# Performance work log

Measured on AMD Instinct MI355X. Metric: run time of the kernel, lower is better.

Reference implementation:

```python
import jax, jax.numpy as jnp
import numpy as np


def setup_inputs() -> dict:
    key = jax.random.key(0)
    ks = jax.random.split(key, 8)
    B, N, K, C_in, M, C_add, C_out = 2, 40000, 16, 64, 16, 3, 128
    in_features = (C_in + C_add) * M  # 1072
    input_features = jax.random.normal(ks[0], (B, N, C_in), dtype=jnp.float32)
    neighbor_inds = jax.random.randint(ks[1], (B, N, K), 0, N, dtype=jnp.int64)
    inverse_neighbors = jax.random.randint(ks[2], (B, N * K), 0, N * K, dtype=jnp.int64)
    inverse_k = jax.random.randint(ks[3], (B, N * K), 0, K, dtype=jnp.int64)
    inverse_idx = jax.random.randint(ks[4], (B, N * K), 0, N, dtype=jnp.int64)
    weightnet = jax.random.normal(ks[5], (B, N, K, M), dtype=jnp.float32)
    additional_features = jax.random.normal(ks[6], (B, N, K, C_add), dtype=jnp.float32)
    bound = 1.0 / np.sqrt(in_features)
    kw, kb = jax.random.split(ks[7])
    linear_weight = jax.random.uniform(kw, (C_out, in_features), dtype=jnp.float32, minval=-bound, maxval=bound)
    linear_bias = jax.random.uniform(kb, (C_out,), dtype=jnp.float32, minval=-bound, maxval=bound)
    return {
        "input_features": input_features,
        "neighbor_inds": neighbor_inds,
        "inverse_neighbors": inverse_neighbors,
        "inverse_k": inverse_k,
        "inverse_idx": inverse_idx,
        "weightnet": weightnet,
        "additional_features": additional_features,
        "linear_weight": linear_weight,
        "linear_bias": linear_bias,
    }


def reference(input_features, neighbor_inds, inverse_neighbors, inverse_k, inverse_idx,
              weightnet, additional_features, linear_weight, linear_bias):
    # inverse_* tensors are only used by the custom CUDA backward; unused here.
    B, N, K = neighbor_inds.shape
    # gather neighbor features: [B, N, K, C_in]
    gathered = jnp.take_along_axis(input_features[:, :, None, :],
                                   neighbor_inds[..., None], axis=1)
    # concat extra per-neighbor features -> [B, N, K, C]
    feats = jnp.concatenate([gathered, additional_features], axis=-1)
    # PConv: [B,N,C,K] @ [B,N,K,M] -> [B,N,C,M] -> flatten to [B,N,C*M]
    pconv = jnp.einsum('bnkc,bnkm->bncm', feats, weightnet)
    pconv = pconv.reshape(B, N, -1)
    # fused linear
    out = jnp.einsum('bnf,of->bno', pconv, linear_weight) + linear_bias
    return out
```

## Files before the change

kernel.cpp:

```cpp
#include <hip/hip_runtime.h>
#include <stdint.h>

typedef unsigned short u16;
typedef short short8 __attribute__((ext_vector_type(8)));
typedef float floatx4 __attribute__((ext_vector_type(4)));

#define NPERB   40000
#define NPTS    80000
#define KNBR    16
#define CIN     64
#define MDIM    16
#define CADD    3
#define CF      (CIN + CADD)
#define COUT    128
#define KF      1072
#define KP      1088
#define NKT     34
#define PTSB    16
#define SLAB    65
#define GRB     32
#define PPB     8
#define LROWB   2192

__device__ __forceinline__ u16 f2bf(float f) {
    union { float f; unsigned int u; } v; v.f = f;
    unsigned int u = v.u;
    return (u16)((u + 0x7FFFu + ((u >> 16) & 1u)) >> 16);
}
__device__ __forceinline__ short8 pack8(floatx4 x, floatx4 y) {
    union { short8 v; u16 a[8]; } u;
    u.a[0] = f2bf(x[0]); u.a[1] = f2bf(x[1]); u.a[2] = f2bf(x[2]); u.a[3] = f2bf(x[3]);
    u.a[4] = f2bf(y[0]); u.a[5] = f2bf(y[1]); u.a[6] = f2bf(y[2]); u.a[7] = f2bf(y[3]);
    return u.v;
}
__device__ __forceinline__ unsigned swz(unsigned chunk) {
    return chunk ^ ((chunk >> 3) & 7u);
}
__device__ __forceinline__ void gload_lds16(const void* g, void* l) {
    __builtin_amdgcn_global_load_lds(
        (const __attribute__((address_space(1))) void*)g,
        (__attribute__((address_space(3))) void*)l, 16, 0, 0);
}

__global__ void prep_lw_kernel(const float* __restrict__ lw, u16* __restrict__ lwp) {
    int i = blockIdx.x * 256 + threadIdx.x;
    if (i >= COUT * KP) return;
    int o = i / KP, f = i - o * KP;
    lwp[i] = (f < KF) ? f2bf(lw[(size_t)o * KF + f]) : (u16)0;
}

__device__ __forceinline__ void emit_point(
    int lane, float av, const float (&fv)[KNBR], const float* wl,
    u16* __restrict__ dst)
{
    const int em = lane & 15, ec = lane >> 4;
    float ev = 0.f;
#pragma unroll
    for (int k = 0; k < KNBR; k++)
        ev += __shfl(av, k * CADD + ec) * wl[k * MDIM + em];
    if (ec == 3) ev = 0.f;
    dst[1024 + lane] = f2bf(ev);

    floatx4 a0 = 0, a1 = 0, a2 = 0, a3 = 0;
#pragma unroll
    for (int k = 0; k < KNBR; k++) {
        const floatx4* w4 = (const floatx4*)(wl + k * MDIM);
        const float fvk = fv[k];
        a0 += fvk * w4[0]; a1 += fvk * w4[1];
        a2 += fvk * w4[2]; a3 += fvk * w4[3];
    }
    *(short8*)(dst + lane * 16)     = pack8(a0, a1);
    *(short8*)(dst + lane * 16 + 8) = pack8(a2, a3);
}

__global__ __launch_bounds__(256) void pconv_kernel(
    const float* __restrict__ inp,
    const int*   __restrict__ nbr,
    const float* __restrict__ wn,
    const float* __restrict__ addl,
    u16* __restrict__ pc)
{
    __shared__ __align__(16) float Wns[PPB * KNBR * MDIM];

    const int wave = threadIdx.x >> 6;
    const int lane = threadIdx.x & 63;
    const int pbase = blockIdx.x * PPB;
    const float* inpb = inp + ((pbase >= NPERB) ? (size_t)NPERB * CIN : 0);

    const int pr0 = wave * 2;
    const int p0  = __builtin_amdgcn_readfirstlane(pbase + pr0);
    const int p1  = p0 + 1;

    float* wl0 = Wns + pr0 * (KNBR * MDIM);
    float* wl1 = wl0 + KNBR * MDIM;
    gload_lds16(wn + (size_t)p0 * (KNBR * MDIM) + lane * 4, wl0);
    gload_lds16(wn + (size_t)p1 * (KNBR * MDIM) + lane * 4, wl1);

    float av0 = (lane < KNBR * CADD) ? addl[(size_t)p0 * (KNBR * CADD) + lane] : 0.f;
    float av1 = (lane < KNBR * CADD) ? addl[(size_t)p1 * (KNBR * CADD) + lane] : 0.f;

    const int* nb0 = nbr + (size_t)p0 * KNBR;
    const int* nb1 = nbr + (size_t)p1 * KNBR;
    int idx0[KNBR], idx1[KNBR];
#pragma unroll
    for (int k = 0; k < KNBR; k++) idx0[k] = nb0[k];
#pragma unroll
    for (int k = 0; k < KNBR; k++) idx1[k] = nb1[k];

    float fv0[KNBR], fv1[KNBR];
#pragma unroll
    for (int k = 0; k < KNBR; k++) fv0[k] = inpb[(size_t)idx0[k] * CIN + lane];
#pragma unroll
    for (int k = 0; k < KNBR; k++) fv1[k] = inpb[(size_t)idx1[k] * CIN + lane];

    asm volatile("s_waitcnt vmcnt(0)" ::: "memory");
    __builtin_amdgcn_sched_barrier(0);

    emit_point(lane, av0, fv0, wl0, pc + (size_t)p0 * KP);
    emit_point(lane, av1, fv1, wl1, pc + (size_t)p1 * KP);
}

__global__ __launch_bounds__(256) void gemm_kernel(
    const u16* __restrict__ pc,
    const u16* __restrict__ lwp,
    const float* __restrict__ bias,
    float* __restrict__ out)
{
    __shared__ __align__(16) u16 As[69 * 512];

    const int wave = threadIdx.x >> 6;
    const int lane = threadIdx.x & 63;
    const int r16 = lane & 15, quad = lane >> 4;
    const int rh = wave >> 1, ch = wave & 1;
    const int row0 = blockIdx.x * GRB;
    const int cb = ch * 64;

    const char* srcb = (const char*)pc + (size_t)row0 * (KP * 2);
#pragma unroll
    for (int j = 0; j < 18; j++) {
        const int w = j * 4 + wave;
        if (w < 69) {
            const unsigned d   = (unsigned)w * 1024u + (unsigned)lane * 16u;
            const unsigned row = d / (unsigned)LROWB;
            const unsigned col = d - row * (unsigned)LROWB;
            gload_lds16(srcb + (size_t)row * 2176u + col,
                        (char*)As + (size_t)w * 1024u);
        }
    }

    const u16* bB0 = lwp + (size_t)(cb + r16) * KP + quad * 8;
    const u16* bB1 = bB0 + (size_t)16 * KP;
    const u16* bB2 = bB0 + (size_t)32 * KP;
    const u16* bB3 = bB0 + (size_t)48 * KP;

    float bv[4];
#pragma unroll
    for (int n = 0; n < 4; n++) bv[n] = bias[cb + n * 16 + r16];

    const u16* aRd = As + (size_t)(rh * 16 + r16) * (LROWB / 2) + quad * 8;

    floatx4 acc[4];
#pragma unroll
    for (int n = 0; n < 4; n++) acc[n] = 0;

    short8 Bq[3][4];
    short8 AR0, AR1;

#define LOADB(t) { \
    Bq[(t) % 3][0] = *(const short8*)(bB0 + (t) * 32); \
    Bq[(t) % 3][1] = *(const short8*)(bB1 + (t) * 32); \
    Bq[(t) % 3][2] = *(const short8*)(bB2 + (t) * 32); \
    Bq[(t) % 3][3] = *(const short8*)(bB3 + (t) * 32); }

    LOADB(0)
    __builtin_amdgcn_sched_barrier(0);
    LOADB(1)
    __builtin_amdgcn_sched_barrier(0);

    asm volatile("s_waitcnt vmcnt(8)" ::: "memory");
    __syncthreads();
    AR0 = *(const short8*)aRd;

#define STEP(kt, NV, NL) { \
    if ((kt) + 2 < NKT) { LOADB((kt) + 2) __builtin_amdgcn_sched_barrier(0); } \
    if ((kt) + 1 < NKT) { \
        if ((((kt) + 1) & 1) == 0) AR0 = *(const short8*)(aRd + ((kt) + 1) * 32); \
        else                       AR1 = *(const short8*)(aRd + ((kt) + 1) * 32); \
    } \
    __builtin_amdgcn_sched_barrier(0); \
    asm volatile("s_waitcnt vmcnt(" #NV ") lgkmcnt(" #NL ")" ::: "memory"); \
    __builtin_amdgcn_sched_barrier(0); \
    _Pragma("unroll") \
    for (int n = 0; n < 4; n++) \
        acc[n] = __builtin_amdgcn_mfma_f32_16x16x32_bf16( \
            (((kt) & 1) == 0) ? AR0 : AR1, Bq[(kt) % 3][n], acc[n], 0, 0, 0); }

    STEP(0, 8, 1)  STEP(1, 8, 1)  STEP(2, 8, 1)  STEP(3, 8, 1)  STEP(4, 8, 1)
    STEP(5, 8, 1)  STEP(6, 8, 1)  STEP(7, 8, 1)  STEP(8, 8, 1)  STEP(9, 8, 1)
    STEP(10, 8, 1) STEP(11, 8, 1) STEP(12, 8, 1) STEP(13, 8, 1) STEP(14, 8, 1)
    STEP(15, 8, 1) STEP(16, 8, 1) STEP(17, 8, 1) STEP(18, 8, 1) STEP(19, 8, 1)
    STEP(20, 8, 1) STEP(21, 8, 1) STEP(22, 8, 1) STEP(23, 8, 1) STEP(24, 8, 1)
    STEP(25, 8, 1) STEP(26, 8, 1) STEP(27, 8, 1) STEP(28, 8, 1) STEP(29, 8, 1)
    STEP(30, 8, 1) STEP(31, 8, 1) STEP(32, 4, 1) STEP(33, 0, 0)

#undef STEP
#undef LOADB

#pragma unroll
    for (int r = 0; r < 4; r++) {
        const size_t row = (size_t)(row0 + rh * 16 + quad * 4 + r) * COUT;
#pragma unroll
        for (int n = 0; n < 4; n++)
            out[row + cb + n * 16 + r16] = acc[n][r] + bv[n];
    }
}

__device__ __forceinline__ void compute_point(
    int pr, int lane, float av, const float (&fv)[KNBR],
    const float* wl, u16* Apc)
{
    const int em = lane & 15, ec = lane >> 4;
    float ev = 0.f;
#pragma unroll
    for (int k = 0; k < KNBR; k++)
        ev += __shfl(av, k * CADD + ec) * wl[k * MDIM + em];
    if (ec == 3) ev = 0.f;
    {
        unsigned kt   = 32 + (lane >> 5);
        unsigned quad = (lane >> 3) & 3;
        unsigned ch   = kt * SLAB + (unsigned)pr * 4 + quad;
        Apc[swz(ch) * 8 + (lane & 7)] = f2bf(ev);
    }
    floatx4 a0 = 0, a1 = 0, a2 = 0, a3 = 0;
#pragma unroll
    for (int k = 0; k < KNBR; k++) {
        const floatx4* w4 = (const floatx4*)(wl + k * MDIM);
        const float fvk = fv[k];
        a0 += fvk * w4[0]; a1 += fvk * w4[1];
        a2 += fvk * w4[2]; a3 += fvk * w4[3];
    }
    {
        unsigned kt = lane >> 1, qb = (lane & 1) * 2;
        unsigned ch = kt * SLAB + (unsigned)pr * 4 + qb;
        *(short8*)&Apc[swz(ch) * 8]     = pack8(a0, a1);
        *(short8*)&Apc[swz(ch + 1) * 8] = pack8(a2, a3);
    }
}

__global__ __launch_bounds__(512, 6) void fused_kernel(
    const float* __restrict__ inp, const int* __restrict__ nbr,
    const float* __restrict__ wn, const float* __restrict__ addl,
    const u16* __restrict__ lwp, const float* __restrict__ bias,
    float* __restrict__ out)
{
    __shared__ __align__(16) u16   Apc[(NKT * SLAB + 8) * 8];
    __shared__ __align__(16) float Wns[PTSB * KNBR * MDIM];

    const int wave = threadIdx.x >> 6;
    const int lane = threadIdx.x & 63;
    const int pbase = blockIdx.x * PTSB;
    const float* inpb = inp + ((pbase >= NPERB) ? (size_t)NPERB * CIN : 0);

    const int pr0 = wave * 2;
    const int p0  = __builtin_amdgcn_readfirstlane(pbase + pr0);
    const int p1  = p0 + 1;

    float* wl0 = Wns + pr0 * (KNBR * MDIM);
    float* wl1 = wl0 + KNBR * MDIM;
    gload_lds16(wn + (size_t)p0 * (KNBR * MDIM) + lane * 4, wl0);
    gload_lds16(wn + (size_t)p1 * (KNBR * MDIM) + lane * 4, wl1);

    float av0 = (lane < KNBR * CADD) ? addl[(size_t)p0 * (KNBR * CADD) + lane] : 0.f;
    float av1 = (lane < KNBR * CADD) ? addl[(size_t)p1 * (KNBR * CADD) + lane] : 0.f;

    const int* nb0 = nbr + (size_t)p0 * KNBR;
    const int* nb1 = nbr + (size_t)p1 * KNBR;
    int idx0[KNBR], idx1[KNBR];
#pragma unroll
    for (int k = 0; k < KNBR; k++) idx0[k] = nb0[k];
#pragma unroll
    for (int k = 0; k < KNBR; k++) idx1[k] = nb1[k];

    float fv0[KNBR], fv1[KNBR];
#pragma unroll
    for (int k = 0; k < KNBR; k++) fv0[k] = inpb[(size_t)idx0[k] * CIN + lane];
#pragma unroll
    for (int k = 0; k < KNBR; k++) fv1[k] = inpb[(size_t)idx1[k] * CIN + lane];

    asm volatile("s_waitcnt vmcnt(0)" ::: "memory");
    __builtin_amdgcn_sched_barrier(0);

    compute_point(pr0,     lane, av0, fv0, wl0, Apc);
    compute_point(pr0 + 1, lane, av1, fv1, wl1, Apc);

    const int r16 = lane & 15, quad = lane >> 4;
    const int c0 = wave * 16;
    const u16* Bp = lwp + (size_t)(c0 + r16) * KP + quad * 8;
    const unsigned abase = (unsigned)r16 * 4 + quad;
    const float bv = bias[c0 + r16];

    __syncthreads();

    floatx4 acc = 0;
#pragma unroll 2
    for (int kt = 0; kt < NKT; kt++) {
        short8 A = *(const short8*)&Apc[swz((unsigned)kt * SLAB + abase) * 8];
        short8 B = *(const short8*)(Bp + kt * 32);
        acc = __builtin_amdgcn_mfma_f32_16x16x32_bf16(A, B, acc, 0, 0, 0);
    }

#pragma unroll
    for (int r = 0; r < 4; r++) {
        const size_t row = (size_t)(pbase + quad * 4 + r) * COUT;
        out[row + c0 + r16] = acc[r] + bv;
    }
}

__global__ __launch_bounds__(256) void fused_fallback_kernel(
    const float* __restrict__ inp, const int* __restrict__ nbr,
    const float* __restrict__ wn, const float* __restrict__ addl,
    const float* __restrict__ lw, const float* __restrict__ bias,
    float* __restrict__ out)
{
    const int p = blockIdx.x;
    const int b = p / NPERB;
    const int tid = threadIdx.x;
    __shared__ float sf[KNBR * CF];
    __shared__ float sw[KNBR * MDIM];
    __shared__ float sp[KF];

    sw[tid] = wn[(size_t)p * (KNBR * MDIM) + tid];
    for (int i = tid; i < KNBR * CIN; i += 256) {
        int k = i >> 6, c = i & 63;
        int idx = nbr[(size_t)p * KNBR + k];
        sf[k * CF + c] = inp[((size_t)b * NPERB + idx) * CIN + c];
    }
    if (tid < KNBR * CADD) {
        int k = tid / CADD, c = tid - k * CADD;
        sf[k * CF + CIN + c] = addl[(size_t)p * (KNBR * CADD) + tid];
    }
    __syncthreads();
    for (int f = tid; f < KF; f += 256) {
        int c = f >> 4, m = f & 15;
        float s = 0;
#pragma unroll
        for (int k = 0; k < KNBR; k++) s += sf[k * CF + c] * sw[k * MDIM + m];
        sp[f] = s;
    }
    __syncthreads();
    const int o = tid >> 1, h = tid & 1;
    float s = 0;
    for (int f = h * (KF / 2); f < (h + 1) * (KF / 2); f++)
        s += sp[f] * lw[(size_t)o * KF + f];
    s += __shfl_xor(s, 1);
    if (h == 0) out[(size_t)p * COUT + o] = s + bias[o];
}

extern "C" void kernel_launch(void* const* d_in, const int* in_sizes, int n_in,
                              void* d_out, int out_size, void* d_ws, size_t ws_size,
                              hipStream_t stream) {
    const float* inp  = (const float*)d_in[0];
    const int*   nbr  = (const int*)d_in[1];
    const float* wn   = (const float*)d_in[5];
    const float* addl = (const float*)d_in[6];
    const float* lw   = (const float*)d_in[7];
    const float* bias = (const float*)d_in[8];
    float* out = (float*)d_out;

    const size_t lw_bytes = (size_t)COUT * KP * sizeof(u16);
    const size_t pc_bytes = (size_t)NPTS * KP * sizeof(u16);

    if (ws_size >= lw_bytes + pc_bytes) {
        u16* pcw = (u16*)d_ws;
        u16* lwp = pcw + (size_t)NPTS * KP;
        prep_lw_kernel<<<(COUT * KP + 255) / 256, 256, 0, stream>>>(lw, lwp);
        pconv_kernel<<<NPTS / PPB, 256, 0, stream>>>(inp, nbr, wn, addl, pcw);
        gemm_kernel<<<NPTS / GRB, 256, 0, stream>>>(pcw, lwp, bias, out);
    } else if (ws_size >= lw_bytes) {
        u16* lwp = (u16*)d_ws;
        prep_lw_kernel<<<(COUT * KP + 255) / 256, 256, 0, stream>>>(lw, lwp);
        fused_kernel<<<NPTS / PTSB, 512, 0, stream>>>(inp, nbr, wn, addl, lwp, bias, out);
    } else {
        fused_fallback_kernel<<<NPTS, 256, 0, stream>>>(inp, nbr, wn, addl, lw, bias, out);
    }
}
```

Before: 383.6 us.

## Store pconv output in MFMA-fragment tiled layout and load A directly from global

The pconv kernel now writes its bf16 output in a 16-row-block tiled layout matching the MFMA A-operand fragment order, so each lane's 8 elements per k-tile are contiguous. The GEMM kernel no longer stages A through LDS with global_load_lds and a barrier. Each wave loads its A fragments straight from global memory in a triple-buffered register pipeline alongside B. The GEMM block grows to 512 threads with one 16x64 tile per wave. This removes LDS traffic and block synchronisation, but adds more outstanding global loads per wave and makes the pconv writes more scattered.

```diff
diff --git a/kernel.cpp b/kernel.cpp
--- a/kernel.cpp
+++ b/kernel.cpp
@@ -18,9 +18,8 @@
 #define NKT     34
 #define PTSB    16
 #define SLAB    65
-#define GRB     32
 #define PPB     8
-#define LROWB   2192
+#define RBSTR   17408
 
 __device__ __forceinline__ u16 f2bf(float f) {
     union { float f; unsigned int u; } v; v.f = f;
@@ -59,7 +58,7 @@
     for (int k = 0; k < KNBR; k++)
         ev += __shfl(av, k * CADD + ec) * wl[k * MDIM + em];
     if (ec == 3) ev = 0.f;
-    dst[1024 + lane] = f2bf(ev);
+    dst[(32 + (lane >> 5)) * 512 + ((lane >> 3) & 3) * 8 + (lane & 7)] = f2bf(ev);
 
     floatx4 a0 = 0, a1 = 0, a2 = 0, a3 = 0;
 #pragma unroll
@@ -69,8 +68,9 @@
         a0 += fvk * w4[0]; a1 += fvk * w4[1];
         a2 += fvk * w4[2]; a3 += fvk * w4[3];
     }
-    *(short8*)(dst + lane * 16)     = pack8(a0, a1);
-    *(short8*)(dst + lane * 16 + 8) = pack8(a2, a3);
+    u16* o = dst + (lane >> 1) * 512 + (lane & 1) * 16;
+    *(short8*)o       = pack8(a0, a1);
+    *(short8*)(o + 8) = pack8(a2, a3);
 }
 
 __global__ __launch_bounds__(256) void pconv_kernel(
@@ -116,38 +116,27 @@
     asm volatile("s_waitcnt vmcnt(0)" ::: "memory");
     __builtin_amdgcn_sched_barrier(0);
 
-    emit_point(lane, av0, fv0, wl0, pc + (size_t)p0 * KP);
-    emit_point(lane, av1, fv1, wl1, pc + (size_t)p1 * KP);
-}
-
-__global__ __launch_bounds__(256) void gemm_kernel(
+    emit_point(lane, av0, fv0, wl0,
+               pc + (size_t)(p0 >> 4) * RBSTR + (p0 & 15) * 32);
+    emit_point(lane, av1, fv1, wl1,
+               pc + (size_t)(p1 >> 4) * RBSTR + (p1 & 15) * 32);
+}
+
+__global__ __launch_bounds__(512, 4) void gemm_kernel(
     const u16* __restrict__ pc,
     const u16* __restrict__ lwp,
     const float* __restrict__ bias,
     float* __restrict__ out)
 {
-    __shared__ __align__(16) u16 As[69 * 512];
-
     const int wave = threadIdx.x >> 6;
     const int lane = threadIdx.x & 63;
     const int r16 = lane & 15, quad = lane >> 4;
-    const int rh = wave >> 1, ch = wave & 1;
-    const int row0 = blockIdx.x * GRB;
-    const int cb = ch * 64;
-
-    const char* srcb = (const char*)pc + (size_t)row0 * (KP * 2);
-#pragma unroll
-    for (int j = 0; j < 18; j++) {
-        const int w = j * 4 + wave;
-        if (w < 69) {
-            const unsigned d   = (unsigned)w * 1024u + (unsigned)lane * 16u;
-            const unsigned row = d / (unsigned)LROWB;
-            const unsigned col = d - row * (unsigned)LROWB;
-            gload_lds16(srcb + (size_t)row * 2176u + col,
-                        (char*)As + (size_t)w * 1024u);
-        }
-    }
-
+    const int wid = blockIdx.x * 8 + wave;
+    const int rb  = wid >> 1;
+    const int cb  = (wid & 1) * 64;
+    const int row0 = rb * 16;
+
+    const u16* aA = pc + (size_t)rb * RBSTR + (((unsigned)r16 << 2) | quad) * 8;
     const u16* bB0 = lwp + (size_t)(cb + r16) * KP + quad * 8;
     const u16* bB1 = bB0 + (size_t)16 * KP;
     const u16* bB2 = bB0 + (size_t)32 * KP;
@@ -156,59 +145,54 @@
     float bv[4];
 #pragma unroll
     for (int n = 0; n < 4; n++) bv[n] = bias[cb + n * 16 + r16];
-
-    const u16* aRd = As + (size_t)(rh * 16 + r16) * (LROWB / 2) + quad * 8;
+    __builtin_amdgcn_sched_barrier(0);
 
     floatx4 acc[4];
 #pragma unroll
     for (int n = 0; n < 4; n++) acc[n] = 0;
 
+    short8 Aq[3];
     short8 Bq[3][4];
-    short8 AR0, AR1;
-
+
+#define LOADA(t) { Aq[(t) % 3] = *(const short8*)(aA + (t) * 512); }
 #define LOADB(t) { \
     Bq[(t) % 3][0] = *(const short8*)(bB0 + (t) * 32); \
     Bq[(t) % 3][1] = *(const short8*)(bB1 + (t) * 32); \
     Bq[(t) % 3][2] = *(const short8*)(bB2 + (t) * 32); \
     Bq[(t) % 3][3] = *(const short8*)(bB3 + (t) * 32); }
 
-    LOADB(0)
-    __builtin_amdgcn_sched_barrier(0);
-    LOADB(1)
-    __builtin_amdgcn_sched_barrier(0);
-
-    asm volatile("s_waitcnt vmcnt(8)" ::: "memory");
-    __syncthreads();
-    AR0 = *(const short8*)aRd;
-
-#define STEP(kt, NV, NL) { \
-    if ((kt) + 2 < NKT) { LOADB((kt) + 2) __builtin_amdgcn_sched_barrier(0); } \
-    if ((kt) + 1 < NKT) { \
-        if ((((kt) + 1) & 1) == 0) AR0 = *(const short8*)(aRd + ((kt) + 1) * 32); \
-        else                       AR1 = *(const short8*)(aRd + ((kt) + 1) * 32); \
+    LOADA(0) LOADB(0)
+    __builtin_amdgcn_sched_barrier(0);
+    LOADA(1) LOADB(1)
+    __builtin_amdgcn_sched_barrier(0);
+
+#define STEP(kt, N) { \
+    if ((kt) + 2 < NKT) { \
+        LOADA((kt) + 2) LOADB((kt) + 2) \
+        __builtin_amdgcn_sched_barrier(0); \
     } \
-    __builtin_amdgcn_sched_barrier(0); \
-    asm volatile("s_waitcnt vmcnt(" #NV ") lgkmcnt(" #NL ")" ::: "memory"); \
+    asm volatile("s_waitcnt vmcnt(" #N ")" ::: "memory"); \
     __builtin_amdgcn_sched_barrier(0); \
     _Pragma("unroll") \
     for (int n = 0; n < 4; n++) \
         acc[n] = __builtin_amdgcn_mfma_f32_16x16x32_bf16( \
-            (((kt) & 1) == 0) ? AR0 : AR1, Bq[(kt) % 3][n], acc[n], 0, 0, 0); }
-
-    STEP(0, 8, 1)  STEP(1, 8, 1)  STEP(2, 8, 1)  STEP(3, 8, 1)  STEP(4, 8, 1)
-    STEP(5, 8, 1)  STEP(6, 8, 1)  STEP(7, 8, 1)  STEP(8, 8, 1)  STEP(9, 8, 1)
-    STEP(10, 8, 1) STEP(11, 8, 1) STEP(12, 8, 1) STEP(13, 8, 1) STEP(14, 8, 1)
-    STEP(15, 8, 1) STEP(16, 8, 1) STEP(17, 8, 1) STEP(18, 8, 1) STEP(19, 8, 1)
-    STEP(20, 8, 1) STEP(21, 8, 1) STEP(22, 8, 1) STEP(23, 8, 1) STEP(24, 8, 1)
-    STEP(25, 8, 1) STEP(26, 8, 1) STEP(27, 8, 1) STEP(28, 8, 1) STEP(29, 8, 1)
-    STEP(30, 8, 1) STEP(31, 8, 1) STEP(32, 4, 1) STEP(33, 0, 0)
+            Aq[(kt) % 3], Bq[(kt) % 3][n], acc[n], 0, 0, 0); }
+
+    STEP(0, 10)  STEP(1, 10)  STEP(2, 10)  STEP(3, 10)  STEP(4, 10)
+    STEP(5, 10)  STEP(6, 10)  STEP(7, 10)  STEP(8, 10)  STEP(9, 10)
+    STEP(10, 10) STEP(11, 10) STEP(12, 10) STEP(13, 10) STEP(14, 10)
+    STEP(15, 10) STEP(16, 10) STEP(17, 10) STEP(18, 10) STEP(19, 10)
+    STEP(20, 10) STEP(21, 10) STEP(22, 10) STEP(23, 10) STEP(24, 10)
+    STEP(25, 10) STEP(26, 10) STEP(27, 10) STEP(28, 10) STEP(29, 10)
+    STEP(30, 10) STEP(31, 10) STEP(32, 5)  STEP(33, 0)
 
 #undef STEP
 #undef LOADB
+#undef LOADA
 
 #pragma unroll
     for (int r = 0; r < 4; r++) {
-        const size_t row = (size_t)(row0 + rh * 16 + quad * 4 + r) * COUT;
+        const size_t row = (size_t)(row0 + quad * 4 + r) * COUT;
 #pragma unroll
         for (int n = 0; n < 4; n++)
             out[row + cb + n * 16 + r16] = acc[n][r] + bv[n];
@@ -375,7 +359,7 @@
         u16* lwp = pcw + (size_t)NPTS * KP;
         prep_lw_kernel<<<(COUT * KP + 255) / 256, 256, 0, stream>>>(lw, lwp);
         pconv_kernel<<<NPTS / PPB, 256, 0, stream>>>(inp, nbr, wn, addl, pcw);
-        gemm_kernel<<<NPTS / GRB, 256, 0, stream>>>(pcw, lwp, bias, out);
+        gemm_kernel<<<(NPTS / 16 * 2) / 8, 512, 0, stream>>>(pcw, lwp, bias, out);
     } else if (ws_size >= lw_bytes) {
         u16* lwp = (u16*)d_ws;
         prep_lw_kernel<<<(COUT * KP + 255) / 256, 256, 0, stream>>>(lw, lwp);
```

Result: slower. 420.3 us (+9.5%).
